# Kernel optimization log

Measured on AMD Instinct MI355X. Metric: run time of the kernel, lower is better.

Reference implementation:

```python
import jax, jax.numpy as jnp
import numpy as np

B, L, K = 8, 1024, 30
NUM_RBF = 16
NPOS = 16
MAXREL = 32
EDGE = 128
EDGE_IN = NPOS + NUM_RBF * 25  # 416

# 25 atom-pair order (ProteinMPNN convention) over atoms [Ca=0, N=1, C=2, O=3, Cb=4]
PAIR_I = np.array([0,1,2,3,4,0,0,0,0,1,1,1,4,4,3,1,2,3,4,2,3,4,2,3,2])
PAIR_J = np.array([0,1,2,3,4,1,2,3,4,2,3,4,2,3,2,0,0,0,0,1,1,1,4,4,3])


def setup_inputs() -> dict:
    key = jax.random.key(0)
    ks = jax.random.split(key, 8)
    X = jax.random.normal(ks[0], (B, L, 4, 3), dtype=jnp.float32) * 3.0
    mask = jnp.ones((B, L), dtype=jnp.float32)
    residue_idx = jnp.arange(B * L, dtype=jnp.int64 if jax.config.jax_enable_x64 else jnp.int32).reshape(B, L)
    S = jax.random.randint(ks[1], (B, L), 0, 21)
    SSE3_seq = jax.random.randint(ks[2], (B, L), 0, 4)
    SSE8_seq = jax.random.randint(ks[3], (B, L), 0, 9)
    W_pos = jax.random.normal(ks[4], (2 * MAXREL + 2, NPOS), dtype=jnp.float32) * 0.02
    b_pos = jnp.zeros((NPOS,), dtype=jnp.float32)
    W_edge = jax.random.normal(ks[5], (EDGE_IN, EDGE), dtype=jnp.float32) * 0.02
    ln_gamma = jnp.ones((EDGE,), dtype=jnp.float32)
    ln_beta = jnp.zeros((EDGE,), dtype=jnp.float32)
    return {"X": X, "mask": mask, "residue_idx": residue_idx, "S": S,
            "SSE3_seq": SSE3_seq, "SSE8_seq": SSE8_seq,
            "W_pos": W_pos, "b_pos": b_pos, "W_edge": W_edge,
            "ln_gamma": ln_gamma, "ln_beta": ln_beta}


def _forward(X, mask, residue_idx, W_pos, b_pos, W_edge, ln_gamma, ln_beta):
    N = X[:, :, 0, :]
    Ca = X[:, :, 1, :]
    C = X[:, :, 2, :]
    O = X[:, :, 3, :]
    b = Ca - N
    c = C - Ca
    a = jnp.cross(b, c)
    Cb = -0.58273431 * a + 0.56802827 * b - 0.54067466 * c + Ca

    # _dist: masked pairwise Ca distances, k smallest
    mask2 = mask[:, :, None] * mask[:, None, :]                      # [B,L,L]
    D = mask2 * jnp.sqrt(jnp.sum((Ca[:, :, None] - Ca[:, None]) ** 2, -1) + 1e-6)
    D_max = jnp.max(D, axis=-1, keepdims=True)
    D_adjust = D + (1.0 - mask2) * D_max
    _, E_idx = jax.lax.top_k(-D_adjust, K)                           # [B,L,K] smallest

    # 25 atom-pair RBFs: gather neighbor atoms, then pairwise atom distances
    atoms = jnp.stack([Ca, N, C, O, Cb], axis=2)                     # [B,L,5,3]
    atoms_nb = jax.vmap(lambda a, i: a[i])(atoms, E_idx)             # [B,L,K,5,3]
    Dp = jnp.sqrt(jnp.sum((atoms[:, :, None, :, None, :] - atoms_nb[:, :, :, None, :, :]) ** 2, -1) + 1e-6)  # [B,L,K,5,5]
    mu = jnp.linspace(2.0, 22.0, NUM_RBF)
    sigma = (22.0 - 2.0) / NUM_RBF
    rbf = jnp.exp(-(((Dp[..., None] - mu) / sigma) ** 2))            # [B,L,K,5,5,R]
    rbf_all = rbf[:, :, :, PAIR_I, PAIR_J, :].reshape(Dp.shape[0], Dp.shape[1], K, 25 * NUM_RBF)

    # positional encodings of relative residue index
    offset = residue_idx[:, :, None] - residue_idx[:, None, :]       # [B,L,L]
    off_nb = jnp.take_along_axis(offset, E_idx, axis=2)              # [B,L,K]
    d = jnp.clip(off_nb + MAXREL, 0, 2 * MAXREL)
    E_pos = W_pos[d] + b_pos                                         # [B,L,K,NPOS]

    E = jnp.concatenate([E_pos, rbf_all], axis=-1) @ W_edge          # [B,L,K,EDGE]
    m = jnp.mean(E, axis=-1, keepdims=True)
    v = jnp.mean((E - m) ** 2, axis=-1, keepdims=True)
    E = (E - m) / jnp.sqrt(v + 1e-5) * ln_gamma + ln_beta
    return E, E_idx


def reference(X, mask, residue_idx, S, SSE3_seq, SSE8_seq, W_pos, b_pos, W_edge, ln_gamma, ln_beta):
    return _forward(X, mask, residue_idx, W_pos, b_pos, W_edge, ln_gamma, ln_beta)
```

## Files before the change

### kernel.cpp

```cpp
#include <hip/hip_runtime.h>

#define BB 8
#define LL 1024
#define KNB 30
#define NUM_RBF 16
#define NPOS 16
#define MAXREL 32
#define EDGE_C 128
#define EDGE_IN 416
#define NKK 26

__constant__ int PAIR_I_d[25] = {0,1,2,3,4,0,0,0,0,1,1,1,4,4,3,1,2,3,4,2,3,4,2,3,2};
__constant__ int PAIR_J_d[25] = {0,1,2,3,4,1,2,3,4,2,3,4,2,3,2,0,0,0,0,1,1,1,4,4,3};

typedef _Float16 half8 __attribute__((ext_vector_type(8)));
typedef float floatx16 __attribute__((ext_vector_type(16)));

__device__ __forceinline__ unsigned long long shfl_down_u64(unsigned long long v, int o) {
    unsigned int lo = (unsigned int)(v & 0xFFFFFFFFull);
    unsigned int hi = (unsigned int)(v >> 32);
    lo = __shfl_down(lo, o);
    hi = __shfl_down(hi, o);
    return ((unsigned long long)hi << 32) | lo;
}
__device__ __forceinline__ unsigned long long shfl_bcast_u64(unsigned long long v, int src) {
    unsigned int lo = (unsigned int)(v & 0xFFFFFFFFull);
    unsigned int hi = (unsigned int)(v >> 32);
    lo = __shfl(lo, src);
    hi = __shfl(hi, src);
    return ((unsigned long long)hi << 32) | lo;
}

__global__ __launch_bounds__(256) void wprep_kernel(const float* __restrict__ W_edge,
                                                    _Float16* __restrict__ WtF) {
    int o = blockIdx.x * 256 + threadIdx.x;
    if (o >= NKK * 4 * 64 * 8) return;
    int j  = o & 7;
    int l  = (o >> 3) & 63;
    int w  = (o >> 9) & 3;
    int kk = o >> 11;
    int k  = (kk << 4) + ((l >> 5) << 3) + j;
    int n  = (w << 5) + (l & 31);
    WtF[o] = (_Float16)W_edge[k * EDGE_C + n];
}

__global__ __launch_bounds__(256) void knn_kernel(const float* __restrict__ X,
                                                  const float* __restrict__ mask,
                                                  float* __restrict__ out_idx) {
    int b  = blockIdx.x >> 8;
    int i0 = (blockIdx.x & 255) * 4;
    int tid = threadIdx.x;
    int lane = tid & 63;
    int wv = tid >> 6;

    __shared__ float sCa[LL * 3];
    __shared__ float sMask[LL];

    for (int j = tid; j < LL; j += 256) {
        int base = (b * LL + j) * 12 + 3;
        sCa[j * 3 + 0] = X[base + 0];
        sCa[j * 3 + 1] = X[base + 1];
        sCa[j * 3 + 2] = X[base + 2];
        sMask[j] = mask[b * LL + j];
    }
    __syncthreads();

    int i = i0 + wv;
    int row = b * LL + i;
    float cax = sCa[i * 3 + 0], cay = sCa[i * 3 + 1], caz = sCa[i * 3 + 2];
    float mi = sMask[i];

    float Dloc[16];
    float dmax = 0.0f;
#pragma unroll
    for (int c = 0; c < 16; ++c) {
        int j = lane + c * 64;
        float dx = cax - sCa[j * 3 + 0];
        float dy = cay - sCa[j * 3 + 1];
        float dz = caz - sCa[j * 3 + 2];
        float m2 = mi * sMask[j];
        float D = m2 * sqrtf(dx * dx + dy * dy + dz * dz + 1e-6f);
        Dloc[c] = D;
        dmax = fmaxf(dmax, D);
    }
    for (int o = 32; o; o >>= 1) dmax = fmaxf(dmax, __shfl_down(dmax, o));
    dmax = __shfl(dmax, 0);

    unsigned long long packed[16];
#pragma unroll
    for (int c = 0; c < 16; ++c) {
        int j = lane + c * 64;
        float m2 = mi * sMask[j];
        float Dadj = Dloc[c] + (1.0f - m2) * dmax;
        unsigned int bits = __float_as_uint(Dadj);
        packed[c] = ((unsigned long long)bits << 32) | (unsigned int)j;
    }

    float* dst = out_idx + (size_t)row * KNB;
    for (int r = 0; r < KNB; ++r) {
        unsigned long long best = packed[0];
#pragma unroll
        for (int c = 1; c < 16; ++c) best = (packed[c] < best) ? packed[c] : best;
        for (int o = 32; o; o >>= 1) {
            unsigned long long other = shfl_down_u64(best, o);
            best = (other < best) ? other : best;
        }
        best = shfl_bcast_u64(best, 0);
        unsigned int jwin = (unsigned int)(best & 0xFFFFFFFFull);
#pragma unroll
        for (int c = 0; c < 16; ++c) {
            if ((unsigned int)(lane + c * 64) == jwin) packed[c] = ~0ull;
        }
        if (lane == 0) dst[r] = (float)jwin;
    }
}

__global__ __launch_bounds__(256) void edge_kernel(const float* __restrict__ X,
                                                   const int* __restrict__ ridx,
                                                   const float* __restrict__ W_pos,
                                                   const float* __restrict__ b_pos,
                                                   const _Float16* __restrict__ WtF,
                                                   const float* __restrict__ gamma,
                                                   const float* __restrict__ beta,
                                                   const float* __restrict__ out_idx,
                                                   float* __restrict__ out_E) {
    int row = blockIdx.x;
    int b = row >> 10;
    int i = row & 1023;
    int tid = threadIdx.x;

    __shared__ __align__(16) char smem[NKK * 64 * 8 * 2];
    _Float16* fA = (_Float16*)smem;
    float* Esh = (float*)smem;

    __shared__ float atoms[31 * 15];
    __shared__ float dist[KNB * 25];
    __shared__ int nbr[KNB];
    __shared__ int dclip[KNB];

    if (tid < KNB) {
        int jn = (int)out_idx[(size_t)row * KNB + tid];
        nbr[tid] = jn;
        int off = ridx[row] - ridx[b * LL + jn];
        int d = off + MAXREL;
        d = d < 0 ? 0 : (d > 2 * MAXREL ? 2 * MAXREL : d);
        dclip[tid] = d;
    }
    __syncthreads();

    if (tid < 31) {
        int r = (tid == 0) ? i : nbr[tid - 1];
        int base = (b * LL + r) * 12;
        float Nx = X[base + 0], Ny = X[base + 1], Nz = X[base + 2];
        float Cax = X[base + 3], Cay = X[base + 4], Caz = X[base + 5];
        float Cx = X[base + 6], Cy = X[base + 7], Cz = X[base + 8];
        float Ox = X[base + 9], Oy = X[base + 10], Oz = X[base + 11];
        float bx = Cax - Nx, by = Cay - Ny, bz = Caz - Nz;
        float cx = Cx - Cax, cy = Cy - Cay, cz = Cz - Caz;
        float ax = by * cz - bz * cy;
        float ay = bz * cx - bx * cz;
        float az = bx * cy - by * cx;
        float Cbx = -0.58273431f * ax + 0.56802827f * bx - 0.54067466f * cx + Cax;
        float Cby = -0.58273431f * ay + 0.56802827f * by - 0.54067466f * cy + Cay;
        float Cbz = -0.58273431f * az + 0.56802827f * bz - 0.54067466f * cz + Caz;
        float* A = &atoms[tid * 15];
        A[0] = Cax; A[1] = Cay; A[2] = Caz;
        A[3] = Nx;  A[4] = Ny;  A[5] = Nz;
        A[6] = Cx;  A[7] = Cy;  A[8] = Cz;
        A[9] = Ox;  A[10] = Oy; A[11] = Oz;
        A[12] = Cbx; A[13] = Cby; A[14] = Cbz;
    }
    __syncthreads();

    for (int idx = tid; idx < KNB * 25; idx += 256) {
        int k = idx / 25;
        int p = idx - k * 25;
        const float* Ai = &atoms[PAIR_I_d[p] * 3];
        const float* Aj = &atoms[(1 + k) * 15 + PAIR_J_d[p] * 3];
        float dx = Ai[0] - Aj[0], dy = Ai[1] - Aj[1], dz = Ai[2] - Aj[2];
        dist[idx] = sqrtf(dx * dx + dy * dy + dz * dz + 1e-6f);
    }
    __syncthreads();

    for (int it = tid; it < 32 * 52; it += 256) {
        int m = it / 52;
        int kg = it - m * 52;
        int k0 = kg * 8;
        half8 v8;
        if (m >= KNB) {
            #pragma unroll
            for (int jj = 0; jj < 8; ++jj) v8[jj] = (_Float16)0.0f;
        } else if (kg < 2) {
            const float* wp = &W_pos[dclip[m] * NPOS + k0];
            const float* bp = &b_pos[k0];
            #pragma unroll
            for (int jj = 0; jj < 8; ++jj) v8[jj] = (_Float16)(wp[jj] + bp[jj]);
        } else {
            int q0 = k0 - NPOS;
            int p = q0 >> 4;
            int r0 = q0 & 15;
            float dd = dist[m * 25 + p];
            #pragma unroll
            for (int jj = 0; jj < 8; ++jj) {
                float mu = 2.0f + (20.0f / 15.0f) * (float)(r0 + jj);
                float x = (dd - mu) * 0.8f;
                v8[jj] = (_Float16)expf(-x * x);
            }
        }
        int pos = ((kg >> 1) * 64 + m + 32 * (kg & 1)) * 8;
        *(half8*)(fA + pos) = v8;
    }
    __syncthreads();

    int wv = tid >> 6;
    int l = tid & 63;
    floatx16 acc;
#pragma unroll
    for (int r = 0; r < 16; ++r) acc[r] = 0.0f;

    const half8* Ap = (const half8*)fA + l;
    const half8* Bp = (const half8*)WtF + wv * 64 + l;
#pragma unroll 4
    for (int kk = 0; kk < NKK; ++kk) {
        half8 a = Ap[kk * 64];
        half8 bfr = Bp[kk * 256];
        acc = __builtin_amdgcn_mfma_f32_32x32x16_f16(a, bfr, acc, 0, 0, 0);
    }
    __syncthreads();

#pragma unroll
    for (int r = 0; r < 16; ++r) {
        int rr = (r & 3) + 8 * (r >> 2) + 4 * (l >> 5);
        Esh[rr * EDGE_C + wv * 32 + (l & 31)] = acc[r];
    }
    __syncthreads();

    int cg = tid & 31;
    int ky = tid >> 5;
    int c0 = cg * 4;
    float gam[4], bet[4];
#pragma unroll
    for (int c = 0; c < 4; ++c) { gam[c] = gamma[c0 + c]; bet[c] = beta[c0 + c]; }

#pragma unroll
    for (int r2 = 0; r2 < 4; ++r2) {
        int e = ky + 8 * r2;
        float v0 = Esh[e * EDGE_C + c0 + 0];
        float v1 = Esh[e * EDGE_C + c0 + 1];
        float v2 = Esh[e * EDGE_C + c0 + 2];
        float v3 = Esh[e * EDGE_C + c0 + 3];
        float s = v0 + v1 + v2 + v3;
        for (int o = 16; o; o >>= 1) s += __shfl_xor(s, o);
        float mean = s * (1.0f / 128.0f);
        float d0 = v0 - mean, d1 = v1 - mean, d2 = v2 - mean, d3 = v3 - mean;
        float vs = d0 * d0 + d1 * d1 + d2 * d2 + d3 * d3;
        for (int o = 16; o; o >>= 1) vs += __shfl_xor(vs, o);
        float inv = 1.0f / sqrtf(vs * (1.0f / 128.0f) + 1e-5f);
        if (e < KNB) {
            float4 o4;
            o4.x = d0 * inv * gam[0] + bet[0];
            o4.y = d1 * inv * gam[1] + bet[1];
            o4.z = d2 * inv * gam[2] + bet[2];
            o4.w = d3 * inv * gam[3] + bet[3];
            *(float4*)(out_E + ((size_t)(row * KNB + e)) * EDGE_C + c0) = o4;
        }
    }
}

extern "C" void kernel_launch(void* const* d_in, const int* in_sizes, int n_in,
                              void* d_out, int out_size, void* d_ws, size_t ws_size,
                              hipStream_t stream) {
    const float* X      = (const float*)d_in[0];
    const float* mask   = (const float*)d_in[1];
    const int*   ridx   = (const int*)d_in[2];
    const float* W_pos  = (const float*)d_in[6];
    const float* b_pos  = (const float*)d_in[7];
    const float* W_edge = (const float*)d_in[8];
    const float* gamma  = (const float*)d_in[9];
    const float* beta   = (const float*)d_in[10];

    float* out_E   = (float*)d_out;
    float* out_idx = out_E + (size_t)BB * LL * KNB * EDGE_C;
    _Float16* WtF  = (_Float16*)d_ws;

    wprep_kernel<<<(NKK * 4 * 64 * 8 + 255) / 256, 256, 0, stream>>>(W_edge, WtF);
    knn_kernel<<<BB * LL / 4, 256, 0, stream>>>(X, mask, out_idx);
    edge_kernel<<<BB * LL, 256, 0, stream>>>(X, ridx, W_pos, b_pos, WtF,
                                             gamma, beta, out_idx, out_E);
}
```

Baseline: 293.1 us.

## Fuse weight prep into kNN launch, use double fmin top-k, compact edge smem

Folds the weight-conversion kernel into extra blocks of the kNN launch, which removes one kernel launch. The kNN selection now encodes each distance and index as a double and uses fmin plus a switch-based kill, instead of 64-bit integer compares with two 32-bit shuffles each. The edge kernel overlays its atoms, dist and index arrays into a single shared buffer to cut LDS use per block. It also restructures RBF generation with a fixed per-thread mapping and the fast __expf, and vectorises the layernorm reads as float4. Risks: double-precision fmin throughput, exactness of the double encoding of float bits times 1024 plus the index, and the accuracy of __expf.

```diff
diff --git a/kernel.cpp b/kernel.cpp
--- a/kernel.cpp
+++ b/kernel.cpp
@@ -9,6 +9,7 @@
 #define EDGE_C 128
 #define EDGE_IN 416
 #define NKK 26
+#define WTF_N (NKK * 4 * 64 * 8)
 
 __constant__ int PAIR_I_d[25] = {0,1,2,3,4,0,0,0,0,1,1,1,4,4,3,1,2,3,4,2,3,4,2,3,2};
 __constant__ int PAIR_J_d[25] = {0,1,2,3,4,1,2,3,4,2,3,4,2,3,2,0,0,0,0,1,1,1,4,4,3};
@@ -16,38 +17,23 @@
 typedef _Float16 half8 __attribute__((ext_vector_type(8)));
 typedef float floatx16 __attribute__((ext_vector_type(16)));
 
-__device__ __forceinline__ unsigned long long shfl_down_u64(unsigned long long v, int o) {
-    unsigned int lo = (unsigned int)(v & 0xFFFFFFFFull);
-    unsigned int hi = (unsigned int)(v >> 32);
-    lo = __shfl_down(lo, o);
-    hi = __shfl_down(hi, o);
-    return ((unsigned long long)hi << 32) | lo;
-}
-__device__ __forceinline__ unsigned long long shfl_bcast_u64(unsigned long long v, int src) {
-    unsigned int lo = (unsigned int)(v & 0xFFFFFFFFull);
-    unsigned int hi = (unsigned int)(v >> 32);
-    lo = __shfl(lo, src);
-    hi = __shfl(hi, src);
-    return ((unsigned long long)hi << 32) | lo;
-}
-
-__global__ __launch_bounds__(256) void wprep_kernel(const float* __restrict__ W_edge,
-                                                    _Float16* __restrict__ WtF) {
-    int o = blockIdx.x * 256 + threadIdx.x;
-    if (o >= NKK * 4 * 64 * 8) return;
-    int j  = o & 7;
-    int l  = (o >> 3) & 63;
-    int w  = (o >> 9) & 3;
-    int kk = o >> 11;
-    int k  = (kk << 4) + ((l >> 5) << 3) + j;
-    int n  = (w << 5) + (l & 31);
-    WtF[o] = (_Float16)W_edge[k * EDGE_C + n];
-}
-
 __global__ __launch_bounds__(256) void knn_kernel(const float* __restrict__ X,
                                                   const float* __restrict__ mask,
-                                                  float* __restrict__ out_idx) {
-    int b  = blockIdx.x >> 8;
+                                                  float* __restrict__ out_idx,
+                                                  const float* __restrict__ W_edge,
+                                                  _Float16* __restrict__ WtF) {
+    if (blockIdx.x >= 2048) {
+        int o = (blockIdx.x - 2048) * 256 + threadIdx.x;
+        if (o < WTF_N) {
+            int j = o & 7, l = (o >> 3) & 63, w = (o >> 9) & 3, kk = o >> 11;
+            int k = (kk << 4) + ((l >> 5) << 3) + j;
+            int n = (w << 5) + (l & 31);
+            WtF[o] = (_Float16)W_edge[k * EDGE_C + n];
+        }
+        return;
+    }
+
+    int b = blockIdx.x >> 8;
     int i0 = (blockIdx.x & 255) * 4;
     int tid = threadIdx.x;
     int lane = tid & 63;
@@ -70,7 +56,7 @@
     float cax = sCa[i * 3 + 0], cay = sCa[i * 3 + 1], caz = sCa[i * 3 + 2];
     float mi = sMask[i];
 
-    float Dloc[16];
+    float Dv[16];
     float dmax = 0.0f;
 #pragma unroll
     for (int c = 0; c < 16; ++c) {
@@ -80,39 +66,65 @@
         float dz = caz - sCa[j * 3 + 2];
         float m2 = mi * sMask[j];
         float D = m2 * sqrtf(dx * dx + dy * dy + dz * dz + 1e-6f);
-        Dloc[c] = D;
+        Dv[c] = D;
         dmax = fmaxf(dmax, D);
     }
     for (int o = 32; o; o >>= 1) dmax = fmaxf(dmax, __shfl_down(dmax, o));
     dmax = __shfl(dmax, 0);
 
-    unsigned long long packed[16];
+    double cand[16];
 #pragma unroll
     for (int c = 0; c < 16; ++c) {
         int j = lane + c * 64;
         float m2 = mi * sMask[j];
-        float Dadj = Dloc[c] + (1.0f - m2) * dmax;
+        float Dadj = Dv[c] + (1.0f - m2) * dmax;
         unsigned int bits = __float_as_uint(Dadj);
-        packed[c] = ((unsigned long long)bits << 32) | (unsigned int)j;
-    }
-
-    float* dst = out_idx + (size_t)row * KNB;
+        cand[c] = fma((double)bits, 1024.0, (double)j);
+    }
+
+    const double KILL = 9.0e15;
+    float myj = 0.0f;
     for (int r = 0; r < KNB; ++r) {
-        unsigned long long best = packed[0];
-#pragma unroll
-        for (int c = 1; c < 16; ++c) best = (packed[c] < best) ? packed[c] : best;
+        double a0 = fmin(cand[0], cand[1]);
+        double a1 = fmin(cand[2], cand[3]);
+        double a2 = fmin(cand[4], cand[5]);
+        double a3 = fmin(cand[6], cand[7]);
+        double a4 = fmin(cand[8], cand[9]);
+        double a5 = fmin(cand[10], cand[11]);
+        double a6 = fmin(cand[12], cand[13]);
+        double a7 = fmin(cand[14], cand[15]);
+        a0 = fmin(a0, a1); a2 = fmin(a2, a3); a4 = fmin(a4, a5); a6 = fmin(a6, a7);
+        a0 = fmin(a0, a2); a4 = fmin(a4, a6);
+        double m = fmin(a0, a4);
         for (int o = 32; o; o >>= 1) {
-            unsigned long long other = shfl_down_u64(best, o);
-            best = (other < best) ? other : best;
-        }
-        best = shfl_bcast_u64(best, 0);
-        unsigned int jwin = (unsigned int)(best & 0xFFFFFFFFull);
-#pragma unroll
-        for (int c = 0; c < 16; ++c) {
-            if ((unsigned int)(lane + c * 64) == jwin) packed[c] = ~0ull;
-        }
-        if (lane == 0) dst[r] = (float)jwin;
-    }
+            double other = __shfl_down(m, o);
+            m = fmin(m, other);
+        }
+        m = __shfl(m, 0);
+        unsigned long long ku = (unsigned long long)m;
+        int jw = __builtin_amdgcn_readfirstlane((int)(ku & 1023));
+        bool own = (lane == (jw & 63));
+        switch (jw >> 6) {
+            case 0:  if (own) cand[0]  = KILL; break;
+            case 1:  if (own) cand[1]  = KILL; break;
+            case 2:  if (own) cand[2]  = KILL; break;
+            case 3:  if (own) cand[3]  = KILL; break;
+            case 4:  if (own) cand[4]  = KILL; break;
+            case 5:  if (own) cand[5]  = KILL; break;
+            case 6:  if (own) cand[6]  = KILL; break;
+            case 7:  if (own) cand[7]  = KILL; break;
+            case 8:  if (own) cand[8]  = KILL; break;
+            case 9:  if (own) cand[9]  = KILL; break;
+            case 10: if (own) cand[10] = KILL; break;
+            case 11: if (own) cand[11] = KILL; break;
+            case 12: if (own) cand[12] = KILL; break;
+            case 13: if (own) cand[13] = KILL; break;
+            case 14: if (own) cand[14] = KILL; break;
+            case 15: if (own) cand[15] = KILL; break;
+        }
+        if (lane == r) myj = (float)jw;
+    }
+    if (lane < KNB) out_idx[(size_t)row * KNB + lane] = myj;
 }
 
 __global__ __launch_bounds__(256) void edge_kernel(const float* __restrict__ X,
@@ -129,14 +141,13 @@
     int i = row & 1023;
     int tid = threadIdx.x;
 
-    __shared__ __align__(16) char smem[NKK * 64 * 8 * 2];
+    __shared__ __align__(16) char smem[29872];
     _Float16* fA = (_Float16*)smem;
     float* Esh = (float*)smem;
-
-    __shared__ float atoms[31 * 15];
-    __shared__ float dist[KNB * 25];
-    __shared__ int nbr[KNB];
-    __shared__ int dclip[KNB];
+    float* atoms = (float*)smem;
+    float* dist = (float*)(smem + 26624);
+    int* nbr = (int*)(smem + 29624);
+    int* dclip = (int*)(smem + 29744);
 
     if (tid < KNB) {
         int jn = (int)out_idx[(size_t)row * KNB + tid];
@@ -182,33 +193,36 @@
     }
     __syncthreads();
 
-    for (int it = tid; it < 32 * 52; it += 256) {
-        int m = it / 52;
-        int kg = it - m * 52;
-        int k0 = kg * 8;
-        half8 v8;
-        if (m >= KNB) {
-            #pragma unroll
-            for (int jj = 0; jj < 8; ++jj) v8[jj] = (_Float16)0.0f;
-        } else if (kg < 2) {
-            const float* wp = &W_pos[dclip[m] * NPOS + k0];
-            const float* bp = &b_pos[k0];
-            #pragma unroll
-            for (int jj = 0; jj < 8; ++jj) v8[jj] = (_Float16)(wp[jj] + bp[jj]);
-        } else {
-            int q0 = k0 - NPOS;
-            int p = q0 >> 4;
-            int r0 = q0 & 15;
-            float dd = dist[m * 25 + p];
-            #pragma unroll
-            for (int jj = 0; jj < 8; ++jj) {
-                float mu = 2.0f + (20.0f / 15.0f) * (float)(r0 + jj);
-                float x = (dd - mu) * 0.8f;
-                v8[jj] = (_Float16)expf(-x * x);
+    {
+        int m = tid & 31;
+        int kgb = tid >> 5;
+#pragma unroll
+        for (int r = 0; r < 7; ++r) {
+            int kg = kgb + 8 * r;
+            if (kg < 52) {
+                half8 v8;
+                if (m >= KNB) {
+#pragma unroll
+                    for (int jj = 0; jj < 8; ++jj) v8[jj] = (_Float16)0.0f;
+                } else if (kg < 2) {
+                    const float* wp = &W_pos[dclip[m] * NPOS + kg * 8];
+                    const float* bp = &b_pos[kg * 8];
+#pragma unroll
+                    for (int jj = 0; jj < 8; ++jj) v8[jj] = (_Float16)(wp[jj] + bp[jj]);
+                } else {
+                    int q0 = kg * 8 - 16;
+                    int p = q0 >> 4;
+                    float t = 0.8f * dist[m * 25 + p] - 1.6f - ((q0 & 8) ? 8.5333336f : 0.0f);
+#pragma unroll
+                    for (int jj = 0; jj < 8; ++jj) {
+                        float x = t - 1.0666667f * (float)jj;
+                        v8[jj] = (_Float16)__expf(-x * x);
+                    }
+                }
+                int pos = ((kg >> 1) * 64 + m + 32 * (kg & 1)) * 8;
+                *(half8*)(fA + pos) = v8;
             }
         }
-        int pos = ((kg >> 1) * 64 + m + 32 * (kg & 1)) * 8;
-        *(half8*)(fA + pos) = v8;
     }
     __syncthreads();
 
@@ -245,14 +259,11 @@
 #pragma unroll
     for (int r2 = 0; r2 < 4; ++r2) {
         int e = ky + 8 * r2;
-        float v0 = Esh[e * EDGE_C + c0 + 0];
-        float v1 = Esh[e * EDGE_C + c0 + 1];
-        float v2 = Esh[e * EDGE_C + c0 + 2];
-        float v3 = Esh[e * EDGE_C + c0 + 3];
-        float s = v0 + v1 + v2 + v3;
+        float4 v = *(const float4*)&Esh[e * EDGE_C + c0];
+        float s = v.x + v.y + v.z + v.w;
         for (int o = 16; o; o >>= 1) s += __shfl_xor(s, o);
         float mean = s * (1.0f / 128.0f);
-        float d0 = v0 - mean, d1 = v1 - mean, d2 = v2 - mean, d3 = v3 - mean;
+        float d0 = v.x - mean, d1 = v.y - mean, d2 = v.z - mean, d3 = v.w - mean;
         float vs = d0 * d0 + d1 * d1 + d2 * d2 + d3 * d3;
         for (int o = 16; o; o >>= 1) vs += __shfl_xor(vs, o);
         float inv = 1.0f / sqrtf(vs * (1.0f / 128.0f) + 1e-5f);
@@ -283,8 +294,8 @@
     float* out_idx = out_E + (size_t)BB * LL * KNB * EDGE_C;
     _Float16* WtF  = (_Float16*)d_ws;
 
-    wprep_kernel<<<(NKK * 4 * 64 * 8 + 255) / 256, 256, 0, stream>>>(W_edge, WtF);
-    knn_kernel<<<BB * LL / 4, 256, 0, stream>>>(X, mask, out_idx);
+    int knn_grid = 2048 + (WTF_N + 255) / 256;
+    knn_kernel<<<knn_grid, 256, 0, stream>>>(X, mask, out_idx, W_edge, WtF);
     edge_kernel<<<BB * LL, 256, 0, stream>>>(X, ridx, W_pos, b_pos, WtF,
                                              gamma, beta, out_idx, out_E);
 }
```

After: 257.2 us. -12.3%, faster.
